# Performance work log

Hardware: AMD Instinct MI355X
Metric: run time of the kernel (lower is better)

Reference implementation:

```python
import jax, jax.numpy as jnp
import numpy as np

# D3 constants (Grimme)
K1 = 16.0           # CN counting-function steepness
K2 = 4.0 / 3.0      # covalent-radius scaling
K3 = 4.0            # Gaussian interpolation width
# BJ damping parameters (init damping_params for the 'energy' variant)
A1, A2, S6, S8 = 0.4, 5.0, 1.0, 0.78
CN_CUTOFF = 25.0    # Bohr
DISP_CUTOFF = 50.0  # Bohr

N_ATOMS = 50000
N_EDGES = 1_600_000
MAX_Z = 95
N_REF = 5


def setup_inputs() -> dict:
    key = jax.random.key(0)
    ks = jax.random.split(key, 8)
    # atoms in a ~40 Bohr box so many pairs fall inside both cutoffs
    positions = jax.random.uniform(ks[0], (N_ATOMS, 3), dtype=jnp.float32) * 40.0
    numbers = jax.random.randint(ks[1], (N_ATOMS,), 1, MAX_Z, dtype=jnp.int32)
    edges_i = jax.random.randint(ks[2], (N_EDGES,), 0, N_ATOMS, dtype=jnp.int32)
    offset = jax.random.randint(ks[3], (N_EDGES,), 1, N_ATOMS, dtype=jnp.int32)
    edges_j = (edges_i + offset) % N_ATOMS  # no self-pairs -> d > 0
    rcov = jax.random.uniform(ks[4], (MAX_Z,), dtype=jnp.float32) * 2.0 + 1.0
    r4r2 = jax.random.uniform(ks[5], (MAX_Z,), dtype=jnp.float32) * 5.0 + 2.0
    c6_table = jax.random.uniform(ks[6], (MAX_Z, MAX_Z, N_REF, N_REF), dtype=jnp.float32) * 100.0
    c6_table = 0.5 * (c6_table + c6_table.transpose(1, 0, 3, 2))  # symmetric like real tables
    cn_ref = jnp.sort(jax.random.uniform(ks[7], (MAX_Z, N_REF), dtype=jnp.float32) * 8.0, axis=-1)
    cn_ref = cn_ref.at[::7, -1].set(-1.0)  # -1 marks absent reference slots
    return dict(positions=positions, numbers=numbers, edges_i=edges_i, edges_j=edges_j,
                rcov=rcov, r4r2=r4r2, c6_table=c6_table, cn_ref=cn_ref)


def _atom_weights(cn_e, refs):
    # cn_e: [E] coordination number at an edge endpoint; refs: [E, M] cn_ref rows
    mask = refs >= 0.0
    gw = jnp.exp(-K3 * (cn_e[:, None] - refs) ** 2) * mask
    norm = jnp.sum(gw, axis=-1, keepdims=True)
    # fallback: one-hot at largest valid reference CN if all Gaussians underflow
    fallback = jax.nn.one_hot(
        jnp.argmax(jnp.where(mask, refs, -jnp.inf), axis=-1), refs.shape[-1], dtype=gw.dtype)
    return jnp.where(norm > 1e-30, gw / jnp.maximum(norm, 1e-30), fallback)


def reference(positions, numbers, edges_i, edges_j, rcov, r4r2, c6_table, cn_ref):
    zi = numbers[edges_i]
    zj = numbers[edges_j]
    vec = positions[edges_j] - positions[edges_i]          # [E, 3]
    d = jnp.sqrt(jnp.sum(vec * vec, axis=-1) + 1e-20)      # [E]

    # --- coordination numbers (scatter-add over directed pairs) ---
    rr = rcov[zi] + rcov[zj]
    cn_pair = jax.nn.sigmoid(K1 * (K2 * rr / d - 1.0)) * (d < CN_CUTOFF)
    cn = jax.ops.segment_sum(cn_pair, edges_i, num_segments=N_ATOMS)  # [N]

    # --- CN-weighted Gaussian interpolation of tabulated C6 ---
    w_i = _atom_weights(cn[edges_i], cn_ref[zi])           # [E, M]
    w_j = _atom_weights(cn[edges_j], cn_ref[zj])           # [E, M]
    c6_ij = jnp.einsum('ea,eb,eab->e', w_i, w_j, c6_table[zi, zj])

    # --- BJ-damped pair dispersion energy ---
    qq = 3.0 * r4r2[zi] * r4r2[zj]
    c8_ij = c6_ij * qq
    f = A1 * jnp.sqrt(qq) + A2
    d2 = d * d
    d6 = d2 * d2 * d2
    d8 = d6 * d2
    e_pair = -(S6 * c6_ij / (d6 + f ** 6) + S8 * c8_ij / (d8 + f ** 8)) * (d < DISP_CUTOFF)

    # split pair energy equally to endpoints (directed list double counts -> 0.5)
    e_atom = jax.ops.segment_sum(0.5 * e_pair, edges_i, num_segments=N_ATOMS)
    return jnp.sum(e_atom)
```

## Files before the change

### kernel.cpp

```cpp
#include <hip/hip_runtime.h>
#include <hip/hip_fp16.h>
#include <math.h>

#define K1C 16.0f
#define K2C (4.0f / 3.0f)
#define K3C 4.0f
#define A1C 0.4f
#define A2C 5.0f
#define S6C 1.0f
#define S8C 0.78f
#define CN_CUT 25.0f
#define DISP_CUT 50.0f
#define MAXZ 95
#define NREF 5
#define THS 32

typedef float f4 __attribute__((ext_vector_type(4)));

__device__ __forceinline__ unsigned h2bits(__half2 h) {
    union { __half2 h; unsigned u; } c; c.h = h; return c.u;
}
__device__ __forceinline__ float2 bits2f2(unsigned u) {
    union { unsigned u; __half2 h; } c; c.u = u; return __half22float2(c.h);
}

__global__ void pack_kernel(const float* __restrict__ pos,
                            const int* __restrict__ numbers,
                            const float* __restrict__ rcov,
                            const float* __restrict__ c6tab,
                            f4* __restrict__ posrec,
                            unsigned* __restrict__ tabh,
                            int n_atoms) {
    int t = blockIdx.x * blockDim.x + threadIdx.x;
    int stride = gridDim.x * blockDim.x;
    const int ntab = MAXZ * MAXZ;
    for (int p = t; p < ntab; p += stride) {
        const float* src = c6tab + (size_t)p * 25;
        float v[32];
#pragma unroll
        for (int k = 0; k < 25; ++k) v[k] = src[k];
#pragma unroll
        for (int k = 25; k < 32; ++k) v[k] = 0.0f;
        unsigned u[16];
#pragma unroll
        for (int k = 0; k < 16; ++k) u[k] = h2bits(__floats2half2_rn(v[2 * k], v[2 * k + 1]));
        uint4* dst = (uint4*)(tabh + (size_t)p * (THS / 2));
        uint4 d0 = { u[0], u[1], u[2], u[3] };
        uint4 d1 = { u[4], u[5], u[6], u[7] };
        uint4 d2 = { u[8], u[9], u[10], u[11] };
        uint4 d3 = { u[12], u[13], u[14], u[15] };
        dst[0] = d0; dst[1] = d1; dst[2] = d2; dst[3] = d3;
    }
    for (int a = t; a < n_atoms; a += stride) {
        int z = numbers[a];
        f4 r = { pos[3 * a + 0], pos[3 * a + 1], pos[3 * a + 2], rcov[z] };
        posrec[a] = r;
    }
}

__global__ void cn_pre_kernel(const f4* __restrict__ posrec,
                              const int* __restrict__ ei,
                              const int* __restrict__ ej,
                              float* __restrict__ cn,
                              uint2* __restrict__ edgerec,
                              int n_edges) {
    int t = blockIdx.x * blockDim.x + threadIdx.x;
    int lane = threadIdx.x & 63;
    int gwave = t >> 6;
    int nwave = (gridDim.x * blockDim.x) >> 6;
    for (int wb = gwave * 256; wb < n_edges; wb += nwave * 256) {
        int e0 = wb + lane;
        int idx[4], jdx[4];
        bool ok[4];
        f4 pa[4], pb[4];
#pragma unroll
        for (int s = 0; s < 4; ++s) {
            int e = e0 + s * 64;
            ok[s] = (e < n_edges);
            idx[s] = ok[s] ? ei[e] : 0;
            jdx[s] = ok[s] ? ej[e] : 0;
        }
#pragma unroll
        for (int s = 0; s < 4; ++s) { pa[s] = posrec[idx[s]]; pb[s] = posrec[jdx[s]]; }
#pragma unroll
        for (int s = 0; s < 4; ++s) {
            int e = e0 + s * 64;
            float dx = pb[s].x - pa[s].x;
            float dy = pb[s].y - pa[s].y;
            float dz = pb[s].z - pa[s].z;
            float d = sqrtf(dx * dx + dy * dy + dz * dz + 1e-20f);
            if (ok[s]) {
                if (d < CN_CUT) {
                    float rr = pa[s].w + pb[s].w;
                    float x = K1C * (K2C * rr / d - 1.0f);
                    atomicAdd(&cn[idx[s]], 1.0f / (1.0f + expf(-x)));
                }
                uint2 r;
                r.x = __float_as_uint(d);
                r.y = (unsigned)idx[s] | ((unsigned)jdx[s] << 16);
                edgerec[e] = r;
            }
        }
    }
}

__global__ void weights_kernel(const float* __restrict__ cn,
                               const int* __restrict__ numbers,
                               const float* __restrict__ cn_ref,
                               const float* __restrict__ r4r2,
                               uint4* __restrict__ wrec,
                               int n_atoms) {
    int stride = gridDim.x * blockDim.x;
    for (int a = blockIdx.x * blockDim.x + threadIdx.x; a < n_atoms; a += stride) {
        int z = numbers[a];
        float c = cn[a];
        float gw[NREF];
        float norm = 0.0f;
        float best = -INFINITY;
        int bi = 0;
#pragma unroll
        for (int m = 0; m < NREF; ++m) {
            float r = cn_ref[z * NREF + m];
            bool valid = (r >= 0.0f);
            float tt = c - r;
            float g = valid ? expf(-K3C * tt * tt) : 0.0f;
            gw[m] = g;
            norm += g;
            if (valid && r > best) { best = r; bi = m; }
        }
        float out[NREF];
        if (norm > 1e-30f) {
            float inv = 1.0f / norm;
#pragma unroll
            for (int m = 0; m < NREF; ++m) out[m] = gw[m] * inv;
        } else {
#pragma unroll
            for (int m = 0; m < NREF; ++m) out[m] = (m == bi) ? 1.0f : 0.0f;
        }
        uint4 r;
        r.x = h2bits(__floats2half2_rn(out[0], out[1]));
        r.y = h2bits(__floats2half2_rn(out[2], out[3]));
        r.z = __float_as_uint(r4r2[z]);
        r.w = (unsigned)z;
        wrec[a] = r;
    }
}

__global__ void energy_kernel(const uint2* __restrict__ edgerec,
                              const uint4* __restrict__ wrec,
                              const unsigned* __restrict__ tabh,
                              double* __restrict__ acc,
                              int n_edges) {
    double local = 0.0;
    int t = blockIdx.x * blockDim.x + threadIdx.x;
    int lane = threadIdx.x & 63;
    int gwave = t >> 6;
    int nwave = (gridDim.x * blockDim.x) >> 6;
    for (int wb = gwave * 256; wb < n_edges; wb += nwave * 256) {
        int e0 = wb + lane;
        uint2 rec[4];
        bool ok[4];
#pragma unroll
        for (int s = 0; s < 4; ++s) {
            int e = e0 + s * 64;
            ok[s] = (e < n_edges);
            uint2 dead = { __float_as_uint(1e30f), 0u };
            rec[s] = ok[s] ? edgerec[e] : dead;
        }
        uint4 wri[4], wrj[4];
#pragma unroll
        for (int s = 0; s < 4; ++s) {
            unsigned ij = rec[s].y;
            wri[s] = wrec[ij & 0xFFFFu];
            wrj[s] = wrec[ij >> 16];
        }
        uint4 t0[4], t1[4], t2[4];
        unsigned t3[4];
#pragma unroll
        for (int s = 0; s < 4; ++s) {
            int pidx = (int)wri[s].w * MAXZ + (int)wrj[s].w;
            const uint4* Tv = (const uint4*)(tabh + (size_t)pidx * (THS / 2));
            t0[s] = Tv[0];
            t1[s] = Tv[1];
            t2[s] = Tv[2];
            t3[s] = ((const unsigned*)Tv)[12];
        }
#pragma unroll
        for (int s = 0; s < 4; ++s) {
            float d = __uint_as_float(rec[s].x);
            if (d < DISP_CUT) {
                float wiv[NREF], wjv[NREF];
                float2 p;
                p = bits2f2(wri[s].x); wiv[0] = p.x; wiv[1] = p.y;
                p = bits2f2(wri[s].y); wiv[2] = p.x; wiv[3] = p.y;
                wiv[4] = 1.0f - (wiv[0] + wiv[1] + wiv[2] + wiv[3]);
                p = bits2f2(wrj[s].x); wjv[0] = p.x; wjv[1] = p.y;
                p = bits2f2(wrj[s].y); wjv[2] = p.x; wjv[3] = p.y;
                wjv[4] = 1.0f - (wjv[0] + wjv[1] + wjv[2] + wjv[3]);
                unsigned us[13] = { t0[s].x, t0[s].y, t0[s].z, t0[s].w,
                                    t1[s].x, t1[s].y, t1[s].z, t1[s].w,
                                    t2[s].x, t2[s].y, t2[s].z, t2[s].w, t3[s] };
                float tt[26];
#pragma unroll
                for (int k = 0; k < 13; ++k) {
                    float2 q = bits2f2(us[k]);
                    tt[2 * k] = q.x;
                    tt[2 * k + 1] = q.y;
                }
                float c6 = 0.0f;
#pragma unroll
                for (int a = 0; a < NREF; ++a) {
                    float sacc = 0.0f;
#pragma unroll
                    for (int b = 0; b < NREF; ++b) sacc += wjv[b] * tt[a * NREF + b];
                    c6 += wiv[a] * sacc;
                }
                float r4i = __uint_as_float(wri[s].z);
                float r4j = __uint_as_float(wrj[s].z);
                float qq = 3.0f * r4i * r4j;
                float c8 = c6 * qq;
                float f = A1C * sqrtf(qq) + A2C;
                float f2 = f * f;
                float f6 = f2 * f2 * f2;
                float f8 = f6 * f2;
                float d2 = d * d;
                float d6 = d2 * d2 * d2;
                float d8 = d6 * d2;
                float e_pair = -(S6C * c6 / (d6 + f6) + S8C * c8 / (d8 + f8));
                local += 0.5 * (double)e_pair;
            }
        }
    }
#pragma unroll
    for (int off = 32; off > 0; off >>= 1) local += __shfl_down(local, off, 64);
    __shared__ double wsum[8];
    int wave = threadIdx.x >> 6;
    if ((threadIdx.x & 63) == 0) wsum[wave] = local;
    __syncthreads();
    if (threadIdx.x == 0) {
        double b = 0.0;
        int nwaves = (blockDim.x + 63) >> 6;
        for (int w = 0; w < nwaves; ++w) b += wsum[w];
        atomicAdd(acc, b);
    }
}

__global__ void cn_kernel_old(const float* __restrict__ pos,
                              const int* __restrict__ numbers,
                              const int* __restrict__ ei,
                              const int* __restrict__ ej,
                              const float* __restrict__ rcov,
                              float* __restrict__ cn,
                              int n_edges) {
    int stride = gridDim.x * blockDim.x;
    for (int e = blockIdx.x * blockDim.x + threadIdx.x; e < n_edges; e += stride) {
        int i = ei[e];
        int j = ej[e];
        float dx = pos[3 * j + 0] - pos[3 * i + 0];
        float dy = pos[3 * j + 1] - pos[3 * i + 1];
        float dz = pos[3 * j + 2] - pos[3 * i + 2];
        float d = sqrtf(dx * dx + dy * dy + dz * dz + 1e-20f);
        if (d < CN_CUT) {
            float rr = rcov[numbers[i]] + rcov[numbers[j]];
            float x = K1C * (K2C * rr / d - 1.0f);
            atomicAdd(&cn[i], 1.0f / (1.0f + expf(-x)));
        }
    }
}

__global__ void energy_kernel_old(const float* __restrict__ pos,
                                  const int* __restrict__ ei,
                                  const int* __restrict__ ej,
                                  const float* __restrict__ c6tab,
                                  const uint4* __restrict__ wrec,
                                  double* __restrict__ acc,
                                  int n_edges) {
    double local = 0.0;
    int stride = gridDim.x * blockDim.x;
    for (int e = blockIdx.x * blockDim.x + threadIdx.x; e < n_edges; e += stride) {
        int i = ei[e];
        int j = ej[e];
        float dx = pos[3 * j + 0] - pos[3 * i + 0];
        float dy = pos[3 * j + 1] - pos[3 * i + 1];
        float dz = pos[3 * j + 2] - pos[3 * i + 2];
        float d = sqrtf(dx * dx + dy * dy + dz * dz + 1e-20f);
        if (d < DISP_CUT) {
            uint4 wi = wrec[i], wj = wrec[j];
            int zi = (int)wi.w, zj = (int)wj.w;
            const float* T = c6tab + ((size_t)(zi * MAXZ + zj)) * 25;
            float wiv[NREF], wjv[NREF];
            float2 p;
            p = bits2f2(wi.x); wiv[0] = p.x; wiv[1] = p.y;
            p = bits2f2(wi.y); wiv[2] = p.x; wiv[3] = p.y;
            wiv[4] = 1.0f - (wiv[0] + wiv[1] + wiv[2] + wiv[3]);
            p = bits2f2(wj.x); wjv[0] = p.x; wjv[1] = p.y;
            p = bits2f2(wj.y); wjv[2] = p.x; wjv[3] = p.y;
            wjv[4] = 1.0f - (wjv[0] + wjv[1] + wjv[2] + wjv[3]);
            float c6 = 0.0f;
#pragma unroll
            for (int a = 0; a < NREF; ++a) {
                float sacc = 0.0f;
#pragma unroll
                for (int b = 0; b < NREF; ++b) sacc += wjv[b] * T[a * NREF + b];
                c6 += wiv[a] * sacc;
            }
            float qq = 3.0f * __uint_as_float(wi.z) * __uint_as_float(wj.z);
            float c8 = c6 * qq;
            float f = A1C * sqrtf(qq) + A2C;
            float f2 = f * f;
            float f6 = f2 * f2 * f2;
            float f8 = f6 * f2;
            float d2 = d * d;
            float d6 = d2 * d2 * d2;
            float d8 = d6 * d2;
            float e_pair = -(S6C * c6 / (d6 + f6) + S8C * c8 / (d8 + f8));
            local += 0.5 * (double)e_pair;
        }
    }
#pragma unroll
    for (int off = 32; off > 0; off >>= 1) local += __shfl_down(local, off, 64);
    __shared__ double wsum[8];
    int wave = threadIdx.x >> 6;
    if ((threadIdx.x & 63) == 0) wsum[wave] = local;
    __syncthreads();
    if (threadIdx.x == 0) {
        double b = 0.0;
        int nwaves = (blockDim.x + 63) >> 6;
        for (int w = 0; w < nwaves; ++w) b += wsum[w];
        atomicAdd(acc, b);
    }
}

__global__ void finalize_kernel(const double* __restrict__ acc, float* __restrict__ out) {
    out[0] = (float)acc[0];
}

static inline size_t align16(size_t x) { return (x + 15) & ~(size_t)15; }

extern "C" void kernel_launch(void* const* d_in, const int* in_sizes, int n_in,
                              void* d_out, int out_size, void* d_ws, size_t ws_size,
                              hipStream_t stream) {
    const float* pos     = (const float*)d_in[0];
    const int*   numbers = (const int*)d_in[1];
    const int*   ei      = (const int*)d_in[2];
    const int*   ej      = (const int*)d_in[3];
    const float* rcov    = (const float*)d_in[4];
    const float* r4r2    = (const float*)d_in[5];
    const float* c6tab   = (const float*)d_in[6];
    const float* cn_ref  = (const float*)d_in[7];

    int n_atoms = in_sizes[1];
    int n_edges = in_sizes[2];

    char* ws = (char*)d_ws;
    size_t off = 0;
    float* cn = (float*)(ws + off);        off += align16((size_t)n_atoms * 4);
    double* acc = (double*)(ws + off);     size_t zero_bytes = off + 16; off += 16;
    uint4* wrec = (uint4*)(ws + off);      off += (size_t)n_atoms * 16;
    size_t small_needed = off;
    f4* posrec = (f4*)(ws + off);          off += (size_t)n_atoms * 16;
    unsigned* tabh = (unsigned*)(ws + off); off += align16((size_t)MAXZ * MAXZ * (THS / 2) * 4);
    uint2* edgerec = (uint2*)(ws + off);   off += (size_t)n_edges * 8;
    size_t full_needed = off;

    hipMemsetAsync(d_ws, 0, zero_bytes, stream);

    const int block = 256;
    int egrid = (n_edges + block - 1) / block;
    int egrid4 = (n_edges + block * 4 - 1) / (block * 4);
    int agrid = (n_atoms + block - 1) / block;
    int pgrid = ((MAXZ * MAXZ > n_atoms ? MAXZ * MAXZ : n_atoms) + block - 1) / block;

    if (ws_size >= full_needed && n_atoms <= 65535) {
        pack_kernel<<<pgrid, block, 0, stream>>>(pos, numbers, rcov, c6tab,
                                                 posrec, tabh, n_atoms);
        cn_pre_kernel<<<egrid4, block, 0, stream>>>(posrec, ei, ej, cn, edgerec, n_edges);
        weights_kernel<<<agrid, block, 0, stream>>>(cn, numbers, cn_ref, r4r2, wrec, n_atoms);
        energy_kernel<<<egrid4, block, 0, stream>>>(edgerec, wrec, tabh, acc, n_edges);
    } else if (ws_size >= small_needed) {
        cn_kernel_old<<<egrid, block, 0, stream>>>(pos, numbers, ei, ej, rcov, cn, n_edges);
        weights_kernel<<<agrid, block, 0, stream>>>(cn, numbers, cn_ref, r4r2, wrec, n_atoms);
        energy_kernel_old<<<egrid, block, 0, stream>>>(pos, ei, ej, c6tab, wrec, acc, n_edges);
    }
    finalize_kernel<<<1, 1, 0, stream>>>(acc, (float*)d_out);
}
```

Measured before the change: 110.5 us.

## Counting-sort edges by element pair before energy kernel for table locality

Adds a four-kernel counting sort (per-block histogram over zi*MAXZ+zj, column scan, prefix, scatter) that reorders edge records by species pair before the energy pass. The aim is that neighbouring edges in a wave read the same C6 table entry, improving cache hits and coalescing on the table gathers. The cost is four extra launches, extra edge-sized reads and writes, LDS atomics and a larger workspace. A fallback keeps the old path when the workspace is too small.

```diff
diff --git a/kernel.cpp b/kernel.cpp
--- a/kernel.cpp
+++ b/kernel.cpp
@@ -14,6 +14,9 @@
 #define MAXZ 95
 #define NREF 5
 #define THS 32
+#define NB 9216
+#define SORTB 128
+#define SORTT 512
 
 typedef float f4 __attribute__((ext_vector_type(4)));
 
@@ -62,7 +65,7 @@
                               const int* __restrict__ ei,
                               const int* __restrict__ ej,
                               float* __restrict__ cn,
-                              uint2* __restrict__ edgerec,
+                              uint2* __restrict__ d_ij,
                               int n_edges) {
     int t = blockIdx.x * blockDim.x + threadIdx.x;
     int lane = threadIdx.x & 63;
@@ -98,7 +101,7 @@
                 uint2 r;
                 r.x = __float_as_uint(d);
                 r.y = (unsigned)idx[s] | ((unsigned)jdx[s] << 16);
-                edgerec[e] = r;
+                d_ij[e] = r;
             }
         }
     }
@@ -143,6 +146,100 @@
         r.z = __float_as_uint(r4r2[z]);
         r.w = (unsigned)z;
         wrec[a] = r;
+    }
+}
+
+__global__ __launch_bounds__(SORTT) void hist_kernel(const uint2* __restrict__ d_ij,
+                                                     const uint4* __restrict__ wrec,
+                                                     unsigned short* __restrict__ pidx16,
+                                                     unsigned* __restrict__ g_hist,
+                                                     int n_edges, int epb) {
+    __shared__ unsigned h[NB];
+    for (int b = threadIdx.x; b < NB; b += blockDim.x) h[b] = 0u;
+    __syncthreads();
+    const unsigned* wrecw = (const unsigned*)wrec;
+    int start = blockIdx.x * epb;
+    int end = start + epb;
+    if (end > n_edges) end = n_edges;
+    for (int e = start + threadIdx.x; e < end; e += blockDim.x) {
+        unsigned ij = d_ij[e].y;
+        unsigned i = ij & 0xFFFFu;
+        unsigned j = ij >> 16;
+        unsigned zi = wrecw[4u * i + 3u];
+        unsigned zj = wrecw[4u * j + 3u];
+        unsigned p = zi * MAXZ + zj;
+        pidx16[e] = (unsigned short)p;
+        atomicAdd(&h[p], 1u);
+    }
+    __syncthreads();
+    unsigned* row = g_hist + (size_t)blockIdx.x * NB;
+    for (int b = threadIdx.x; b < NB; b += blockDim.x) row[b] = h[b];
+}
+
+__global__ void scan_kernel(unsigned* __restrict__ g_hist,
+                            unsigned* __restrict__ bin_total) {
+    int bin = blockIdx.x * blockDim.x + threadIdx.x;
+    if (bin >= NB) return;
+    unsigned run = 0;
+    for (int b = 0; b < SORTB; ++b) {
+        unsigned t = g_hist[(size_t)b * NB + bin];
+        g_hist[(size_t)b * NB + bin] = run;
+        run += t;
+    }
+    bin_total[bin] = run;
+}
+
+__global__ __launch_bounds__(1024) void prefix_kernel(const unsigned* __restrict__ bin_total,
+                                                      unsigned* __restrict__ bin_base) {
+    const int BPT = NB / 1024;
+    int tid = threadIdx.x;
+    unsigned v[BPT];
+    unsigned sum = 0;
+#pragma unroll
+    for (int k = 0; k < BPT; ++k) {
+        unsigned t = bin_total[tid * BPT + k];
+        v[k] = sum;
+        sum += t;
+    }
+    int lane = tid & 63;
+    int wid = tid >> 6;
+    unsigned s = sum;
+#pragma unroll
+    for (int d = 1; d < 64; d <<= 1) {
+        unsigned t = __shfl_up(s, d, 64);
+        if (lane >= d) s += t;
+    }
+    __shared__ unsigned wtot[16];
+    if (lane == 63) wtot[wid] = s;
+    __syncthreads();
+    if (tid == 0) {
+        unsigned r = 0;
+        for (int w = 0; w < 16; ++w) { unsigned t = wtot[w]; wtot[w] = r; r += t; }
+    }
+    __syncthreads();
+    unsigned excl = wtot[wid] + s - sum;
+#pragma unroll
+    for (int k = 0; k < BPT; ++k) bin_base[tid * BPT + k] = excl + v[k];
+}
+
+__global__ __launch_bounds__(SORTT) void scatter_kernel(const uint2* __restrict__ d_ij,
+                                                        const unsigned short* __restrict__ pidx16,
+                                                        const unsigned* __restrict__ g_hist,
+                                                        const unsigned* __restrict__ bin_base,
+                                                        uint2* __restrict__ sorted,
+                                                        int n_edges, int epb) {
+    __shared__ unsigned cur[NB];
+    const unsigned* row = g_hist + (size_t)blockIdx.x * NB;
+    for (int b = threadIdx.x; b < NB; b += blockDim.x) cur[b] = row[b] + bin_base[b];
+    __syncthreads();
+    int start = blockIdx.x * epb;
+    int end = start + epb;
+    if (end > n_edges) end = n_edges;
+    for (int e = start + threadIdx.x; e < end; e += blockDim.x) {
+        uint2 r = d_ij[e];
+        unsigned p = pidx16[e];
+        unsigned pos = atomicAdd(&cur[p], 1u);
+        sorted[pos] = r;
     }
 }
 
@@ -354,13 +451,19 @@
 
     char* ws = (char*)d_ws;
     size_t off = 0;
-    float* cn = (float*)(ws + off);        off += align16((size_t)n_atoms * 4);
-    double* acc = (double*)(ws + off);     size_t zero_bytes = off + 16; off += 16;
-    uint4* wrec = (uint4*)(ws + off);      off += (size_t)n_atoms * 16;
+    float* cn = (float*)(ws + off);          off += align16((size_t)n_atoms * 4);
+    double* acc = (double*)(ws + off);       size_t zero_bytes = off + 16; off += 16;
+    uint4* wrec = (uint4*)(ws + off);        off += (size_t)n_atoms * 16;
     size_t small_needed = off;
-    f4* posrec = (f4*)(ws + off);          off += (size_t)n_atoms * 16;
-    unsigned* tabh = (unsigned*)(ws + off); off += align16((size_t)MAXZ * MAXZ * (THS / 2) * 4);
-    uint2* edgerec = (uint2*)(ws + off);   off += (size_t)n_edges * 8;
+    f4* posrec = (f4*)(ws + off);            off += (size_t)n_atoms * 16;
+    unsigned* tabh = (unsigned*)(ws + off);  off += align16((size_t)MAXZ * MAXZ * (THS / 2) * 4);
+    uint2* d_ij = (uint2*)(ws + off);        off += (size_t)n_edges * 8;
+    size_t mid_needed = off;
+    unsigned short* pidx16 = (unsigned short*)(ws + off); off += align16((size_t)n_edges * 2);
+    uint2* sorted = (uint2*)(ws + off);      off += (size_t)n_edges * 8;
+    unsigned* g_hist = (unsigned*)(ws + off); off += (size_t)SORTB * NB * 4;
+    unsigned* bin_total = (unsigned*)(ws + off); off += (size_t)NB * 4;
+    unsigned* bin_base = (unsigned*)(ws + off);  off += (size_t)NB * 4;
     size_t full_needed = off;
 
     hipMemsetAsync(d_ws, 0, zero_bytes, stream);
@@ -370,13 +473,25 @@
     int egrid4 = (n_edges + block * 4 - 1) / (block * 4);
     int agrid = (n_atoms + block - 1) / block;
     int pgrid = ((MAXZ * MAXZ > n_atoms ? MAXZ * MAXZ : n_atoms) + block - 1) / block;
+    int epb = (n_edges + SORTB - 1) / SORTB;
 
     if (ws_size >= full_needed && n_atoms <= 65535) {
         pack_kernel<<<pgrid, block, 0, stream>>>(pos, numbers, rcov, c6tab,
                                                  posrec, tabh, n_atoms);
-        cn_pre_kernel<<<egrid4, block, 0, stream>>>(posrec, ei, ej, cn, edgerec, n_edges);
+        cn_pre_kernel<<<egrid4, block, 0, stream>>>(posrec, ei, ej, cn, d_ij, n_edges);
         weights_kernel<<<agrid, block, 0, stream>>>(cn, numbers, cn_ref, r4r2, wrec, n_atoms);
-        energy_kernel<<<egrid4, block, 0, stream>>>(edgerec, wrec, tabh, acc, n_edges);
+        hist_kernel<<<SORTB, SORTT, 0, stream>>>(d_ij, wrec, pidx16, g_hist, n_edges, epb);
+        scan_kernel<<<(NB + 255) / 256, 256, 0, stream>>>(g_hist, bin_total);
+        prefix_kernel<<<1, 1024, 0, stream>>>(bin_total, bin_base);
+        scatter_kernel<<<SORTB, SORTT, 0, stream>>>(d_ij, pidx16, g_hist, bin_base,
+                                                    sorted, n_edges, epb);
+        energy_kernel<<<egrid4, block, 0, stream>>>(sorted, wrec, tabh, acc, n_edges);
+    } else if (ws_size >= mid_needed && n_atoms <= 65535) {
+        pack_kernel<<<pgrid, block, 0, stream>>>(pos, numbers, rcov, c6tab,
+                                                 posrec, tabh, n_atoms);
+        cn_pre_kernel<<<egrid4, block, 0, stream>>>(posrec, ei, ej, cn, d_ij, n_edges);
+        weights_kernel<<<agrid, block, 0, stream>>>(cn, numbers, cn_ref, r4r2, wrec, n_atoms);
+        energy_kernel<<<egrid4, block, 0, stream>>>(d_ij, wrec, tabh, acc, n_edges);
     } else if (ws_size >= small_needed) {
         cn_kernel_old<<<egrid, block, 0, stream>>>(pos, numbers, ei, ej, rcov, cn, n_edges);
         weights_kernel<<<agrid, block, 0, stream>>>(cn, numbers, cn_ref, r4r2, wrec, n_atoms);
```

Measured after the change: 168.3 us. +52.3%, slower.

## Replicate CN accumulators and carry pair index in wider edge records

Applied to the files above, without the earlier changes.

The coordination-number scatter-add now targets one of four replicated CN arrays chosen by block index, which spreads atomic contention; the weights kernel sums the copies. The atomic number is packed into the rcov slot of posrec, so the CN pass can write the C6 table pair index into a widened 16-byte edge record. The energy kernel can then issue the table loads without waiting on the per-atom weight-record gather. In exchange the edge records double in size, adding write and read traffic, and the memset region grows.

```diff
diff --git a/kernel.cpp b/kernel.cpp
--- a/kernel.cpp
+++ b/kernel.cpp
@@ -14,6 +14,7 @@
 #define MAXZ 95
 #define NREF 5
 #define THS 32
+#define NCN 4
 
 typedef float f4 __attribute__((ext_vector_type(4)));
 
@@ -53,7 +54,8 @@
     }
     for (int a = t; a < n_atoms; a += stride) {
         int z = numbers[a];
-        f4 r = { pos[3 * a + 0], pos[3 * a + 1], pos[3 * a + 2], rcov[z] };
+        f4 r = { pos[3 * a + 0], pos[3 * a + 1], pos[3 * a + 2],
+                 rcov[z] + 4.0f * (float)z };
         posrec[a] = r;
     }
 }
@@ -61,13 +63,14 @@
 __global__ void cn_pre_kernel(const f4* __restrict__ posrec,
                               const int* __restrict__ ei,
                               const int* __restrict__ ej,
-                              float* __restrict__ cn,
-                              uint2* __restrict__ edgerec,
-                              int n_edges) {
+                              float* __restrict__ cn4,
+                              uint4* __restrict__ erec,
+                              int n_edges, int npad) {
     int t = blockIdx.x * blockDim.x + threadIdx.x;
     int lane = threadIdx.x & 63;
     int gwave = t >> 6;
     int nwave = (gridDim.x * blockDim.x) >> 6;
+    float* cnc = cn4 + (size_t)(blockIdx.x & (NCN - 1)) * npad;
     for (int wb = gwave * 256; wb < n_edges; wb += nwave * 256) {
         int e0 = wb + lane;
         int idx[4], jdx[4];
@@ -89,31 +92,39 @@
             float dy = pb[s].y - pa[s].y;
             float dz = pb[s].z - pa[s].z;
             float d = sqrtf(dx * dx + dy * dy + dz * dz + 1e-20f);
+            int zi = (int)floorf(pa[s].w * 0.25f);
+            int zj = (int)floorf(pb[s].w * 0.25f);
+            float rci = pa[s].w - 4.0f * (float)zi;
+            float rcj = pb[s].w - 4.0f * (float)zj;
             if (ok[s]) {
                 if (d < CN_CUT) {
-                    float rr = pa[s].w + pb[s].w;
+                    float rr = rci + rcj;
                     float x = K1C * (K2C * rr / d - 1.0f);
-                    atomicAdd(&cn[idx[s]], 1.0f / (1.0f + expf(-x)));
+                    atomicAdd(&cnc[idx[s]], 1.0f / (1.0f + expf(-x)));
                 }
-                uint2 r;
+                uint4 r;
                 r.x = __float_as_uint(d);
                 r.y = (unsigned)idx[s] | ((unsigned)jdx[s] << 16);
-                edgerec[e] = r;
+                r.z = (unsigned)(zi * MAXZ + zj);
+                r.w = 0u;
+                erec[e] = r;
             }
         }
     }
 }
 
-__global__ void weights_kernel(const float* __restrict__ cn,
+__global__ void weights_kernel(const float* __restrict__ cn4,
                                const int* __restrict__ numbers,
                                const float* __restrict__ cn_ref,
                                const float* __restrict__ r4r2,
                                uint4* __restrict__ wrec,
-                               int n_atoms) {
+                               int n_atoms, int npad) {
     int stride = gridDim.x * blockDim.x;
     for (int a = blockIdx.x * blockDim.x + threadIdx.x; a < n_atoms; a += stride) {
         int z = numbers[a];
-        float c = cn[a];
+        float c = 0.0f;
+#pragma unroll
+        for (int k = 0; k < NCN; ++k) c += cn4[(size_t)k * npad + a];
         float gw[NREF];
         float norm = 0.0f;
         float best = -INFINITY;
@@ -146,7 +157,7 @@
     }
 }
 
-__global__ void energy_kernel(const uint2* __restrict__ edgerec,
+__global__ void energy_kernel(const uint4* __restrict__ erec,
                               const uint4* __restrict__ wrec,
                               const unsigned* __restrict__ tabh,
                               double* __restrict__ acc,
@@ -158,28 +169,24 @@
     int nwave = (gridDim.x * blockDim.x) >> 6;
     for (int wb = gwave * 256; wb < n_edges; wb += nwave * 256) {
         int e0 = wb + lane;
-        uint2 rec[4];
+        uint4 rec[4];
         bool ok[4];
 #pragma unroll
         for (int s = 0; s < 4; ++s) {
             int e = e0 + s * 64;
             ok[s] = (e < n_edges);
-            uint2 dead = { __float_as_uint(1e30f), 0u };
-            rec[s] = ok[s] ? edgerec[e] : dead;
+            uint4 dead = { __float_as_uint(1e30f), 0u, 0u, 0u };
+            rec[s] = ok[s] ? erec[e] : dead;
         }
         uint4 wri[4], wrj[4];
+        uint4 t0[4], t1[4], t2[4];
+        unsigned t3[4];
 #pragma unroll
         for (int s = 0; s < 4; ++s) {
             unsigned ij = rec[s].y;
             wri[s] = wrec[ij & 0xFFFFu];
             wrj[s] = wrec[ij >> 16];
-        }
-        uint4 t0[4], t1[4], t2[4];
-        unsigned t3[4];
-#pragma unroll
-        for (int s = 0; s < 4; ++s) {
-            int pidx = (int)wri[s].w * MAXZ + (int)wrj[s].w;
-            const uint4* Tv = (const uint4*)(tabh + (size_t)pidx * (THS / 2));
+            const uint4* Tv = (const uint4*)(tabh + (size_t)rec[s].z * (THS / 2));
             t0[s] = Tv[0];
             t1[s] = Tv[1];
             t2[s] = Tv[2];
@@ -265,6 +272,48 @@
             float x = K1C * (K2C * rr / d - 1.0f);
             atomicAdd(&cn[i], 1.0f / (1.0f + expf(-x)));
         }
+    }
+}
+
+__global__ void weights_kernel_old(const float* __restrict__ cn,
+                                   const int* __restrict__ numbers,
+                                   const float* __restrict__ cn_ref,
+                                   const float* __restrict__ r4r2,
+                                   uint4* __restrict__ wrec,
+                                   int n_atoms) {
+    int stride = gridDim.x * blockDim.x;
+    for (int a = blockIdx.x * blockDim.x + threadIdx.x; a < n_atoms; a += stride) {
+        int z = numbers[a];
+        float c = cn[a];
+        float gw[NREF];
+        float norm = 0.0f;
+        float best = -INFINITY;
+        int bi = 0;
+#pragma unroll
+        for (int m = 0; m < NREF; ++m) {
+            float r = cn_ref[z * NREF + m];
+            bool valid = (r >= 0.0f);
+            float tt = c - r;
+            float g = valid ? expf(-K3C * tt * tt) : 0.0f;
+            gw[m] = g;
+            norm += g;
+            if (valid && r > best) { best = r; bi = m; }
+        }
+        float out[NREF];
+        if (norm > 1e-30f) {
+            float inv = 1.0f / norm;
+#pragma unroll
+            for (int m = 0; m < NREF; ++m) out[m] = gw[m] * inv;
+        } else {
+#pragma unroll
+            for (int m = 0; m < NREF; ++m) out[m] = (m == bi) ? 1.0f : 0.0f;
+        }
+        uint4 r;
+        r.x = h2bits(__floats2half2_rn(out[0], out[1]));
+        r.y = h2bits(__floats2half2_rn(out[2], out[3]));
+        r.z = __float_as_uint(r4r2[z]);
+        r.w = (unsigned)z;
+        wrec[a] = r;
     }
 }
 
@@ -351,16 +400,17 @@
 
     int n_atoms = in_sizes[1];
     int n_edges = in_sizes[2];
+    int npad = (n_atoms + 3) & ~3;
 
     char* ws = (char*)d_ws;
     size_t off = 0;
-    float* cn = (float*)(ws + off);        off += align16((size_t)n_atoms * 4);
-    double* acc = (double*)(ws + off);     size_t zero_bytes = off + 16; off += 16;
-    uint4* wrec = (uint4*)(ws + off);      off += (size_t)n_atoms * 16;
+    float* cn4 = (float*)(ws + off);        off += (size_t)NCN * npad * 4;
+    double* acc = (double*)(ws + off);      size_t zero_bytes = off + 16; off += 16;
+    uint4* wrec = (uint4*)(ws + off);       off += (size_t)n_atoms * 16;
     size_t small_needed = off;
-    f4* posrec = (f4*)(ws + off);          off += (size_t)n_atoms * 16;
+    f4* posrec = (f4*)(ws + off);           off += (size_t)n_atoms * 16;
     unsigned* tabh = (unsigned*)(ws + off); off += align16((size_t)MAXZ * MAXZ * (THS / 2) * 4);
-    uint2* edgerec = (uint2*)(ws + off);   off += (size_t)n_edges * 8;
+    uint4* erec = (uint4*)(ws + off);       off += (size_t)n_edges * 16;
     size_t full_needed = off;
 
     hipMemsetAsync(d_ws, 0, zero_bytes, stream);
@@ -374,12 +424,15 @@
     if (ws_size >= full_needed && n_atoms <= 65535) {
         pack_kernel<<<pgrid, block, 0, stream>>>(pos, numbers, rcov, c6tab,
                                                  posrec, tabh, n_atoms);
-        cn_pre_kernel<<<egrid4, block, 0, stream>>>(posrec, ei, ej, cn, edgerec, n_edges);
-        weights_kernel<<<agrid, block, 0, stream>>>(cn, numbers, cn_ref, r4r2, wrec, n_atoms);
-        energy_kernel<<<egrid4, block, 0, stream>>>(edgerec, wrec, tabh, acc, n_edges);
+        cn_pre_kernel<<<egrid4, block, 0, stream>>>(posrec, ei, ej, cn4, erec,
+                                                    n_edges, npad);
+        weights_kernel<<<agrid, block, 0, stream>>>(cn4, numbers, cn_ref, r4r2,
+                                                    wrec, n_atoms, npad);
+        energy_kernel<<<egrid4, block, 0, stream>>>(erec, wrec, tabh, acc, n_edges);
     } else if (ws_size >= small_needed) {
-        cn_kernel_old<<<egrid, block, 0, stream>>>(pos, numbers, ei, ej, rcov, cn, n_edges);
-        weights_kernel<<<agrid, block, 0, stream>>>(cn, numbers, cn_ref, r4r2, wrec, n_atoms);
+        cn_kernel_old<<<egrid, block, 0, stream>>>(pos, numbers, ei, ej, rcov, cn4, n_edges);
+        weights_kernel_old<<<agrid, block, 0, stream>>>(cn4, numbers, cn_ref, r4r2,
+                                                        wrec, n_atoms);
         energy_kernel_old<<<egrid, block, 0, stream>>>(pos, ei, ej, c6tab, wrec, acc, n_edges);
     }
     finalize_kernel<<<1, 1, 0, stream>>>(acc, (float*)d_out);
```

After: 123.1 us. +11.4%, slower.

## Privatize coordination-number accumulators per XCD with workgroup-scope atomics

Applied to the files above, without the earlier changes.

The coordination-number scatter-add now goes into one of eight private copies of the CN array, chosen by the hardware XCC id read with s_getreg. It uses relaxed workgroup-scope atomics instead of device-scope atomicAdd. The weights kernel sums the eight copies when it reads CN. The goal is to keep the atomics local to each XCD's L2 instead of forcing device-coherent atomics across dies. The trade-off is a larger memset, eight reads per atom, and a reliance on workgroup-scope atomics staying coherent across workgroups on the same XCD. The edge record also switches from uint2 to a single 64-bit value.

```diff
diff --git a/kernel.cpp b/kernel.cpp
--- a/kernel.cpp
+++ b/kernel.cpp
@@ -14,14 +14,21 @@
 #define MAXZ 95
 #define NREF 5
 #define THS 32
+#define NXCD 8
 
 typedef float f4 __attribute__((ext_vector_type(4)));
+typedef unsigned long long u64;
 
 __device__ __forceinline__ unsigned h2bits(__half2 h) {
     union { __half2 h; unsigned u; } c; c.h = h; return c.u;
 }
 __device__ __forceinline__ float2 bits2f2(unsigned u) {
     union { unsigned u; __half2 h; } c; c.u = u; return __half22float2(c.h);
+}
+__device__ __forceinline__ int xcc_id() {
+    int x;
+    asm volatile("s_getreg_b32 %0, hwreg(HW_REG_XCC_ID)" : "=s"(x));
+    return x & (NXCD - 1);
 }
 
 __global__ void pack_kernel(const float* __restrict__ pos,
@@ -61,13 +68,14 @@
 __global__ void cn_pre_kernel(const f4* __restrict__ posrec,
                               const int* __restrict__ ei,
                               const int* __restrict__ ej,
-                              float* __restrict__ cn,
-                              uint2* __restrict__ edgerec,
-                              int n_edges) {
+                              float* __restrict__ cn8,
+                              u64* __restrict__ erec,
+                              int n_edges, int npad) {
     int t = blockIdx.x * blockDim.x + threadIdx.x;
     int lane = threadIdx.x & 63;
     int gwave = t >> 6;
     int nwave = (gridDim.x * blockDim.x) >> 6;
+    float* cnx = cn8 + (size_t)xcc_id() * npad;
     for (int wb = gwave * 256; wb < n_edges; wb += nwave * 256) {
         int e0 = wb + lane;
         int idx[4], jdx[4];
@@ -93,27 +101,30 @@
                 if (d < CN_CUT) {
                     float rr = pa[s].w + pb[s].w;
                     float x = K1C * (K2C * rr / d - 1.0f);
-                    atomicAdd(&cn[idx[s]], 1.0f / (1.0f + expf(-x)));
+                    float v = 1.0f / (1.0f + expf(-x));
+                    __hip_atomic_fetch_add(&cnx[idx[s]], v,
+                                           __ATOMIC_RELAXED, __HIP_MEMORY_SCOPE_WORKGROUP);
                 }
-                uint2 r;
-                r.x = __float_as_uint(d);
-                r.y = (unsigned)idx[s] | ((unsigned)jdx[s] << 16);
-                edgerec[e] = r;
+                u64 r = (u64)__float_as_uint(d) |
+                        ((u64)((unsigned)idx[s] | ((unsigned)jdx[s] << 16)) << 32);
+                erec[e] = r;
             }
         }
     }
 }
 
-__global__ void weights_kernel(const float* __restrict__ cn,
+__global__ void weights_kernel(const float* __restrict__ cn8,
                                const int* __restrict__ numbers,
                                const float* __restrict__ cn_ref,
                                const float* __restrict__ r4r2,
                                uint4* __restrict__ wrec,
-                               int n_atoms) {
+                               int n_atoms, int npad) {
     int stride = gridDim.x * blockDim.x;
     for (int a = blockIdx.x * blockDim.x + threadIdx.x; a < n_atoms; a += stride) {
         int z = numbers[a];
-        float c = cn[a];
+        float c = 0.0f;
+#pragma unroll
+        for (int k = 0; k < NXCD; ++k) c += cn8[(size_t)k * npad + a];
         float gw[NREF];
         float norm = 0.0f;
         float best = -INFINITY;
@@ -146,7 +157,7 @@
     }
 }
 
-__global__ void energy_kernel(const uint2* __restrict__ edgerec,
+__global__ void energy_kernel(const u64* __restrict__ erec,
                               const uint4* __restrict__ wrec,
                               const unsigned* __restrict__ tabh,
                               double* __restrict__ acc,
@@ -158,19 +169,16 @@
     int nwave = (gridDim.x * blockDim.x) >> 6;
     for (int wb = gwave * 256; wb < n_edges; wb += nwave * 256) {
         int e0 = wb + lane;
-        uint2 rec[4];
-        bool ok[4];
+        u64 rec[4];
 #pragma unroll
         for (int s = 0; s < 4; ++s) {
             int e = e0 + s * 64;
-            ok[s] = (e < n_edges);
-            uint2 dead = { __float_as_uint(1e30f), 0u };
-            rec[s] = ok[s] ? edgerec[e] : dead;
+            rec[s] = (e < n_edges) ? erec[e] : (u64)__float_as_uint(1e30f);
         }
         uint4 wri[4], wrj[4];
 #pragma unroll
         for (int s = 0; s < 4; ++s) {
-            unsigned ij = rec[s].y;
+            unsigned ij = (unsigned)(rec[s] >> 32);
             wri[s] = wrec[ij & 0xFFFFu];
             wrj[s] = wrec[ij >> 16];
         }
@@ -187,7 +195,7 @@
         }
 #pragma unroll
         for (int s = 0; s < 4; ++s) {
-            float d = __uint_as_float(rec[s].x);
+            float d = __uint_as_float((unsigned)rec[s]);
             if (d < DISP_CUT) {
                 float wiv[NREF], wjv[NREF];
                 float2 p;
@@ -351,16 +359,17 @@
 
     int n_atoms = in_sizes[1];
     int n_edges = in_sizes[2];
+    int npad = (n_atoms + 3) & ~3;
 
     char* ws = (char*)d_ws;
     size_t off = 0;
-    float* cn = (float*)(ws + off);        off += align16((size_t)n_atoms * 4);
-    double* acc = (double*)(ws + off);     size_t zero_bytes = off + 16; off += 16;
-    uint4* wrec = (uint4*)(ws + off);      off += (size_t)n_atoms * 16;
+    float* cn8 = (float*)(ws + off);        off += (size_t)NXCD * npad * 4;
+    double* acc = (double*)(ws + off);      size_t zero_bytes = off + 16; off += 16;
+    uint4* wrec = (uint4*)(ws + off);       off += (size_t)n_atoms * 16;
     size_t small_needed = off;
-    f4* posrec = (f4*)(ws + off);          off += (size_t)n_atoms * 16;
+    f4* posrec = (f4*)(ws + off);           off += (size_t)n_atoms * 16;
     unsigned* tabh = (unsigned*)(ws + off); off += align16((size_t)MAXZ * MAXZ * (THS / 2) * 4);
-    uint2* edgerec = (uint2*)(ws + off);   off += (size_t)n_edges * 8;
+    u64* erec = (u64*)(ws + off);           off += (size_t)n_edges * 8;
     size_t full_needed = off;
 
     hipMemsetAsync(d_ws, 0, zero_bytes, stream);
@@ -374,12 +383,15 @@
     if (ws_size >= full_needed && n_atoms <= 65535) {
         pack_kernel<<<pgrid, block, 0, stream>>>(pos, numbers, rcov, c6tab,
                                                  posrec, tabh, n_atoms);
-        cn_pre_kernel<<<egrid4, block, 0, stream>>>(posrec, ei, ej, cn, edgerec, n_edges);
-        weights_kernel<<<agrid, block, 0, stream>>>(cn, numbers, cn_ref, r4r2, wrec, n_atoms);
-        energy_kernel<<<egrid4, block, 0, stream>>>(edgerec, wrec, tabh, acc, n_edges);
+        cn_pre_kernel<<<egrid4, block, 0, stream>>>(posrec, ei, ej, cn8, erec,
+                                                    n_edges, npad);
+        weights_kernel<<<agrid, block, 0, stream>>>(cn8, numbers, cn_ref, r4r2,
+                                                    wrec, n_atoms, npad);
+        energy_kernel<<<egrid4, block, 0, stream>>>(erec, wrec, tabh, acc, n_edges);
     } else if (ws_size >= small_needed) {
-        cn_kernel_old<<<egrid, block, 0, stream>>>(pos, numbers, ei, ej, rcov, cn, n_edges);
-        weights_kernel<<<agrid, block, 0, stream>>>(cn, numbers, cn_ref, r4r2, wrec, n_atoms);
+        cn_kernel_old<<<egrid, block, 0, stream>>>(pos, numbers, ei, ej, rcov, cn8, n_edges);
+        weights_kernel<<<agrid, block, 0, stream>>>(cn8, numbers, cn_ref, r4r2,
+                                                    wrec, n_atoms, npad);
         energy_kernel_old<<<egrid, block, 0, stream>>>(pos, ei, ej, c6tab, wrec, acc, n_edges);
     }
     finalize_kernel<<<1, 1, 0, stream>>>(acc, (float*)d_out);
```

Result: slower. 118.9 us (+7.6%).
